# Kernel tuning notes

Hardware: AMD Instinct MI355X
Metric: run time of the kernel (lower is better)

Reference implementation:

```python
import jax, jax.numpy as jnp
import numpy as np

B, T, C, N = 64, 1024, 2, 128


def setup_inputs() -> dict:
    key = jax.random.key(0)
    k1, k2, k3, k4, k5 = jax.random.split(key, 5)
    return {
        "emissions": jax.random.normal(k1, (B, T, C, N), dtype=jnp.float32),
        "lengths": jax.random.randint(k2, (B,), T // 2, T + 1),
        "transitions": jax.random.normal(k3, (1, C, N, N), dtype=jnp.float32) * 0.01,
        "start_transitions": jax.random.normal(k4, (1, C, N), dtype=jnp.float32) * 0.01,
        "end_transitions": jax.random.normal(k5, (1, C, N), dtype=jnp.float32) * 0.01,
    }


def reference(emissions, lengths, transitions, start_transitions, end_transitions):
    """CRF log-partition over ragged batch (equivalent to torchlatent's
    log-semiring tree-reduce over PackedSequence, expressed as a masked scan).
    emissions: [B,T,C,N], lengths: [B], transitions: [1,C,N,N],
    start/end_transitions: [1,C,N]. Returns log Z: [B,C].
    """
    trans = transitions[0]              # [C,N,N], shared across time
    alpha0 = start_transitions[0][None] + emissions[:, 0]  # [B,C,N]

    def step(alpha, inp):
        emit, t = inp                   # emit: [B,C,N]
        # log-semiring bmm: logsumexp over previous tag axis
        scores = alpha[:, :, :, None] + trans[None] + emit[:, :, None, :]  # [B,C,N,N]
        new = jax.nn.logsumexp(scores, axis=2)                             # [B,C,N]
        alpha = jnp.where((t < lengths)[:, None, None], new, alpha)
        return alpha, None

    emits = jnp.moveaxis(emissions[:, 1:], 1, 0)  # [T-1,B,C,N]
    alpha, _ = jax.lax.scan(step, alpha0, (emits, jnp.arange(1, T)))
    return jax.nn.logsumexp(alpha + end_transitions[0][None], axis=-1)  # [B,C]
```

## Files before the change

kernel.cpp:

```cpp
#include <hip/hip_runtime.h>

#define BB 64
#define TT 1024
#define CC 2
#define NN 128

#define REP16(M) M(0)M(1)M(2)M(3)M(4)M(5)M(6)M(7)M(8)M(9)M(10)M(11)M(12)M(13)M(14)M(15)

static __device__ __forceinline__ unsigned f2bf(float x) {
    const unsigned u = __float_as_uint(x);
    return (u + 0x7FFFu + ((u >> 16) & 1u)) >> 16;
}
static __device__ __forceinline__ unsigned pk2(float lo, float hi) {
    return f2bf(lo) | (f2bf(hi) << 16);
}

#define DOT(acc, pp, ee) \
    asm("v_dot2_f32_bf16 %0, %1, %2, %0" : "+v"(acc) : "v"(pp), "v"(ee));

#define E_INIT(k) \
    uint4 ea##k, eb##k; \
    ea##k.x = pk2(__expf(tr[(8*(k)+0)*NN + j0]), __expf(tr[(8*(k)+1)*NN + j0])); \
    ea##k.y = pk2(__expf(tr[(8*(k)+2)*NN + j0]), __expf(tr[(8*(k)+3)*NN + j0])); \
    ea##k.z = pk2(__expf(tr[(8*(k)+4)*NN + j0]), __expf(tr[(8*(k)+5)*NN + j0])); \
    ea##k.w = pk2(__expf(tr[(8*(k)+6)*NN + j0]), __expf(tr[(8*(k)+7)*NN + j0])); \
    eb##k.x = pk2(__expf(tr[(8*(k)+0)*NN + j1]), __expf(tr[(8*(k)+1)*NN + j1])); \
    eb##k.y = pk2(__expf(tr[(8*(k)+2)*NN + j1]), __expf(tr[(8*(k)+3)*NN + j1])); \
    eb##k.z = pk2(__expf(tr[(8*(k)+4)*NN + j1]), __expf(tr[(8*(k)+5)*NN + j1])); \
    eb##k.w = pk2(__expf(tr[(8*(k)+6)*NN + j1]), __expf(tr[(8*(k)+7)*NN + j1]));

#define E_PIN(k) \
    asm volatile("" : "+v"(ea##k.x), "+v"(ea##k.y), "+v"(ea##k.z), "+v"(ea##k.w)); \
    asm volatile("" : "+v"(eb##k.x), "+v"(eb##k.y), "+v"(eb##k.z), "+v"(eb##k.w));

#define MV(k) { const uint4 q = pb[(k)]; \
    DOT(a0, q.x, ea##k.x) DOT(a1, q.y, ea##k.y) \
    DOT(a2, q.z, ea##k.z) DOT(a3, q.w, ea##k.w) \
    DOT(b0, q.x, eb##k.x) DOT(b1, q.y, eb##k.y) \
    DOT(b2, q.z, eb##k.z) DOT(b3, q.w, eb##k.w) }

__global__ void
__attribute__((amdgpu_flat_work_group_size(64, 64), amdgpu_waves_per_eu(1, 1)))
crf_logz_kernel(const float* __restrict__ emissions,
                const int* __restrict__ lengths,
                const float* __restrict__ transitions,
                const float* __restrict__ start_trans,
                const float* __restrict__ end_trans,
                float* __restrict__ out)
{
    const int bc = blockIdx.x;
    const int b  = bc >> 1;
    const int c  = bc & 1;
    const int L  = threadIdx.x;
    const int j0 = 2 * L;
    const int j1 = 2 * L + 1;

    __shared__ __align__(16) unsigned pbuf[2][64];

    const float* tr = transitions + c * NN * NN;
    REP16(E_INIT)
    REP16(E_PIN)

    const int len  = lengths[b];
    const int tmax = len - 1;

    const float* emisb = emissions + ((size_t)b * TT * CC + c) * NN;

    float alpha0 = start_trans[c * NN + j0] + emisb[j0];
    float alpha1 = start_trans[c * NN + j1] + emisb[j1];

    const int t1 = (1 < tmax) ? 1 : tmax, t2 = (2 < tmax) ? 2 : tmax;
    float2 ecur = *(const float2*)&emisb[(size_t)t1 * (CC * NN) + j0];
    float2 enx  = *(const float2*)&emisb[(size_t)t2 * (CC * NN) + j0];

    for (int t = 1; t < len; ++t) {
        const int tp = (t + 2 <= tmax) ? (t + 2) : tmax;
        const float2 el = *(const float2*)&emisb[(size_t)tp * (CC * NN) + j0];

        const float shift =
            __int_as_float(__builtin_amdgcn_readfirstlane(__float_as_int(alpha0)));
        pbuf[t & 1][L] = pk2(__expf(alpha0 - shift), __expf(alpha1 - shift));
        __builtin_amdgcn_wave_barrier();

        const uint4* __restrict__ pb = (const uint4*)pbuf[t & 1];
        float a0 = 0.f, a1 = 0.f, a2 = 0.f, a3 = 0.f;
        float b0 = 0.f, b1 = 0.f, b2 = 0.f, b3 = 0.f;
        REP16(MV)

        alpha0 = shift + __logf((a0 + a1) + (a2 + a3)) + ecur.x;
        alpha1 = shift + __logf((b0 + b1) + (b2 + b3)) + ecur.y;
        ecur = enx; enx = el;
    }

    const float x0 = alpha0 + end_trans[c * NN + j0];
    const float x1 = alpha1 + end_trans[c * NN + j1];
    float m = fmaxf(x0, x1);
    #pragma unroll
    for (int off = 32; off > 0; off >>= 1)
        m = fmaxf(m, __shfl_xor(m, off));
    float s = __expf(x0 - m) + __expf(x1 - m);
    #pragma unroll
    for (int off = 32; off > 0; off >>= 1)
        s += __shfl_xor(s, off);
    if (L == 0) out[b * CC + c] = m + __logf(s);
}

extern "C" void kernel_launch(void* const* d_in, const int* in_sizes, int n_in,
                              void* d_out, int out_size, void* d_ws, size_t ws_size,
                              hipStream_t stream) {
    const float* emissions   = (const float*)d_in[0];
    const int*   lengths     = (const int*)d_in[1];
    const float* transitions = (const float*)d_in[2];
    const float* start_t     = (const float*)d_in[3];
    const float* end_t       = (const float*)d_in[4];
    float* out = (float*)d_out;

    crf_logz_kernel<<<BB * CC, 64, 0, stream>>>(
        emissions, lengths, transitions, start_t, end_t, out);
}
```

Measured before the change: 582.2 us.

## Carry alpha in scaled linear domain to remove per-step exp/log

Keeps the forward variable as scaled probabilities plus a scalar log-scale S instead of log-alpha. Each step computes the emission exps off the critical path, then normalizes the dot products by a reciprocal of lane 0's sum. Only one log per step feeds S, and the next probabilities are written straight to a single LDS buffer. This shortens the serial dependency chain per timestep, at the cost of relying on lane-0 normalization staying numerically safe, and the launch attribute is also changed to request 256 VGPRs.

```diff
diff --git a/kernel.cpp b/kernel.cpp
--- a/kernel.cpp
+++ b/kernel.cpp
@@ -13,6 +13,9 @@
 }
 static __device__ __forceinline__ unsigned pk2(float lo, float hi) {
     return f2bf(lo) | (f2bf(hi) << 16);
+}
+static __device__ __forceinline__ float rfl(float x) {
+    return __int_as_float(__builtin_amdgcn_readfirstlane(__float_as_int(x)));
 }
 
 #define DOT(acc, pp, ee) \
@@ -40,7 +43,7 @@
     DOT(b2, q.z, eb##k.z) DOT(b3, q.w, eb##k.w) }
 
 __global__ void
-__attribute__((amdgpu_flat_work_group_size(64, 64), amdgpu_waves_per_eu(1, 1)))
+__attribute__((amdgpu_flat_work_group_size(64, 64), amdgpu_num_vgpr(256)))
 crf_logz_kernel(const float* __restrict__ emissions,
                 const int* __restrict__ lengths,
                 const float* __restrict__ transitions,
@@ -55,7 +58,7 @@
     const int j0 = 2 * L;
     const int j1 = 2 * L + 1;
 
-    __shared__ __align__(16) unsigned pbuf[2][64];
+    __shared__ __align__(16) unsigned pbuf[64];
 
     const float* tr = transitions + c * NN * NN;
     REP16(E_INIT)
@@ -66,8 +69,12 @@
 
     const float* emisb = emissions + ((size_t)b * TT * CC + c) * NN;
 
-    float alpha0 = start_trans[c * NN + j0] + emisb[j0];
-    float alpha1 = start_trans[c * NN + j1] + emisb[j1];
+    const float ai0 = start_trans[c * NN + j0] + emisb[j0];
+    const float ai1 = start_trans[c * NN + j1] + emisb[j1];
+    float S   = rfl(ai0);
+    float s0f = __expf(ai0 - S);
+    float s1f = __expf(ai1 - S);
+    pbuf[L] = pk2(s0f, s1f);
 
     const int t1 = (1 < tmax) ? 1 : tmax, t2 = (2 < tmax) ? 2 : tmax;
     float2 ecur = *(const float2*)&emisb[(size_t)t1 * (CC * NN) + j0];
@@ -77,32 +84,37 @@
         const int tp = (t + 2 <= tmax) ? (t + 2) : tmax;
         const float2 el = *(const float2*)&emisb[(size_t)tp * (CC * NN) + j0];
 
-        const float shift =
-            __int_as_float(__builtin_amdgcn_readfirstlane(__float_as_int(alpha0)));
-        pbuf[t & 1][L] = pk2(__expf(alpha0 - shift), __expf(alpha1 - shift));
-        __builtin_amdgcn_wave_barrier();
+        const float e0 = rfl(ecur.x);
+        const float x0 = __expf(ecur.x - e0);
+        const float x1 = __expf(ecur.y - e0);
 
-        const uint4* __restrict__ pb = (const uint4*)pbuf[t & 1];
+        const uint4* __restrict__ pb = (const uint4*)pbuf;
         float a0 = 0.f, a1 = 0.f, a2 = 0.f, a3 = 0.f;
         float b0 = 0.f, b1 = 0.f, b2 = 0.f, b3 = 0.f;
         REP16(MV)
 
-        alpha0 = shift + __logf((a0 + a1) + (a2 + a3)) + ecur.x;
-        alpha1 = shift + __logf((b0 + b1) + (b2 + b3)) + ecur.y;
+        const float dj0 = (a0 + a1) + (a2 + a3);
+        const float dj1 = (b0 + b1) + (b2 + b3);
+        const float dz  = rfl(dj0);
+        float r;
+        asm("v_rcp_f32 %0, %1" : "=v"(r) : "v"(dz));
+
+        s0f = (dj0 * r) * x0;
+        s1f = (dj1 * r) * x1;
+        pbuf[L] = pk2(s0f, s1f);
+        __builtin_amdgcn_wave_barrier();
+
+        S += e0 + __logf(dz);
+
         ecur = enx; enx = el;
     }
 
-    const float x0 = alpha0 + end_trans[c * NN + j0];
-    const float x1 = alpha1 + end_trans[c * NN + j1];
-    float m = fmaxf(x0, x1);
+    float z = s0f * __expf(end_trans[c * NN + j0])
+            + s1f * __expf(end_trans[c * NN + j1]);
     #pragma unroll
     for (int off = 32; off > 0; off >>= 1)
-        m = fmaxf(m, __shfl_xor(m, off));
-    float s = __expf(x0 - m) + __expf(x1 - m);
-    #pragma unroll
-    for (int off = 32; off > 0; off >>= 1)
-        s += __shfl_xor(s, off);
-    if (L == 0) out[b * CC + c] = m + __logf(s);
+        z += __shfl_xor(z, off);
+    if (L == 0) out[b * CC + c] = S + __logf(z);
 }
 
 extern "C" void kernel_launch(void* const* d_in, const int* in_sizes, int n_in,
```

After: 813.0 us. +39.6%, slower.
